# Optimization experiments

Hardware: AMD Instinct MI355X
Metric: run time of the kernel (lower is better)

The kernel has to match this reference:

```python
import jax, jax.numpy as jnp
import numpy as np

B, S, D_IN, D_OUT, H = 4, 2048, 768, 768, 12
DH = D_OUT // H


def setup_inputs() -> dict:
    key = jax.random.key(0)
    ks = jax.random.split(key, 6)
    x = jax.random.normal(ks[0], (B, S, D_IN), dtype=jnp.float32)
    # causal mask: True above the diagonal means "masked out" (filled with -inf)
    mask = jnp.triu(jnp.ones((S, S), dtype=bool), k=1)
    sc = 1.0 / np.sqrt(D_IN)
    Wq = jax.random.normal(ks[1], (D_IN, D_OUT), dtype=jnp.float32) * sc
    Wk = jax.random.normal(ks[2], (D_IN, D_OUT), dtype=jnp.float32) * sc
    Wv = jax.random.normal(ks[3], (D_IN, D_OUT), dtype=jnp.float32) * sc
    Wo = jax.random.normal(ks[4], (D_OUT, D_OUT), dtype=jnp.float32) * (1.0 / np.sqrt(D_OUT))
    bo = jnp.zeros((D_OUT,), dtype=jnp.float32)
    return {"input_tensor": x, "mask": mask, "Wq": Wq, "Wk": Wk, "Wv": Wv, "Wo": Wo, "bo": bo}


def reference(input_tensor, mask, Wq, Wk, Wv, Wo, bo):
    b, n, _ = input_tensor.shape
    # projections -> [b, h, n, dh]
    q = (input_tensor @ Wq).reshape(b, n, H, DH).transpose(0, 2, 1, 3)
    k = (input_tensor @ Wk).reshape(b, n, H, DH).transpose(0, 2, 1, 3)
    v = (input_tensor @ Wv).reshape(b, n, H, DH).transpose(0, 2, 1, 3)
    # scores [b, h, n, n]
    scores = jnp.einsum('bhqd,bhkd->bhqk', q, k)
    scores = jnp.where(mask[:n, :n], -jnp.inf, scores)
    attn = jax.nn.softmax(scores / np.sqrt(DH), axis=-1)
    ctx = jnp.einsum('bhqk,bhkd->bhqd', attn, v)
    ctx = ctx.transpose(0, 2, 1, 3).reshape(b, n, D_OUT)
    return ctx @ Wo + bo
```

## Files before the change

kernel.cpp:

```cpp
#include <hip/hip_runtime.h>
#include <hip/hip_bf16.h>
#include <math.h>

typedef __attribute__((ext_vector_type(4))) float f32x4;
typedef __attribute__((ext_vector_type(8))) short s16x8;
typedef __attribute__((ext_vector_type(8))) unsigned short u16x8;

#define B_ 4
#define S_ 2048
#define DIN 768
#define DOUT 768
#define H_ 12
#define DH_ 64
#define M_ (B_*S_)

__device__ __forceinline__ unsigned short f2bf(float f) {
  union { float f; unsigned u; } v; v.f = f;
  unsigned r = v.u + 0x7fffu + ((v.u >> 16) & 1u);
  return (unsigned short)(r >> 16);
}


__global__ __launch_bounds__(256) void prep(
    const float* __restrict__ X, unsigned short* __restrict__ Xb,
    const float* __restrict__ W0, const float* __restrict__ W1,
    const float* __restrict__ W2, const float* __restrict__ W3,
    unsigned short* __restrict__ Wt)
{
  __shared__ float t[32][33];
  const int bid = blockIdx.x;
  if (bid < 3072) {
    size_t i = ((size_t)bid * 256 + threadIdx.x) * 8;
    float4 a = *(const float4*)&X[i];
    float4 b = *(const float4*)&X[i + 4];
    u16x8 v;
    v[0] = f2bf(a.x); v[1] = f2bf(a.y); v[2] = f2bf(a.z); v[3] = f2bf(a.w);
    v[4] = f2bf(b.x); v[5] = f2bf(b.y); v[6] = f2bf(b.z); v[7] = f2bf(b.w);
    *(u16x8*)&Xb[i] = v;
  } else {
    const int t4 = bid - 3072;
    const int z = t4 / 576, rem = t4 - z * 576;
    const int ky = rem / 24, nx = rem - ky * 24;
    const float* W = z == 0 ? W0 : z == 1 ? W1 : z == 2 ? W2 : W3;
    unsigned short* Out = Wt + (size_t)z * DOUT * DIN;
    const int n0 = nx * 32, k0 = ky * 32;
    const int tx = threadIdx.x & 31, ty = threadIdx.x >> 5;
#pragma unroll
    for (int i = 0; i < 32; i += 8)
      t[ty + i][tx] = W[(size_t)(k0 + ty + i) * DOUT + n0 + tx];
    __syncthreads();
#pragma unroll
    for (int i = 0; i < 32; i += 8)
      Out[(size_t)(n0 + ty + i) * DIN + k0 + tx] = f2bf(t[tx][ty + i]);
  }
}


#define BKC 64
#define TILE_E (128 * BKC)

__device__ __forceinline__ void stage_tile(
    const unsigned short* __restrict__ g, int row0, int k0,
    unsigned short* lds, int tid)
{
#pragma unroll
  for (int it = 0; it < 4; ++it) {
    int s = it * 256 + tid;
    int row = s >> 3, sc = s & 7;
    int gc = sc ^ (row & 7);
    const unsigned short* gsrc = g + (size_t)(row0 + row) * 768 + k0 + gc * 8;
    unsigned short* dst = lds + (size_t)(it * 256 + (tid & ~63)) * 8;
    __builtin_amdgcn_global_load_lds(
        (const __attribute__((address_space(1))) void*)gsrc,
        (__attribute__((address_space(3))) void*)dst, 16, 0, 0);
  }
}

__device__ __forceinline__ void gemm_core(
    const unsigned short* __restrict__ A, const unsigned short* __restrict__ Bt,
    int m0, int n0, unsigned short* As, unsigned short* Bs,
    f32x4 acc[4][4], int tid)
{
  const int lane = tid & 63;
  const int col_l = lane & 15, quad = lane >> 4;
  const int w = tid >> 6;
  const int wm = (w & 1) * 64, wn = (w >> 1) * 64;

  stage_tile(A, m0, 0, As, tid);
  stage_tile(Bt, n0, 0, Bs, tid);

#pragma unroll 2
  for (int k0 = 0; k0 < 768; k0 += BKC) {
    const int cur = (k0 >> 6) & 1;
    const unsigned short* Asb = As + cur * TILE_E;
    const unsigned short* Bsb = Bs + cur * TILE_E;
    if (k0 + BKC < 768) {
      stage_tile(A, m0, k0 + BKC, As + (cur ^ 1) * TILE_E, tid);
      stage_tile(Bt, n0, k0 + BKC, Bs + (cur ^ 1) * TILE_E, tid);
      asm volatile("s_waitcnt vmcnt(8)" ::: "memory");
    } else {
      asm volatile("s_waitcnt vmcnt(0)" ::: "memory");
    }
    __builtin_amdgcn_s_barrier();

#pragma unroll
    for (int kk = 0; kk < 2; ++kk) {
      s16x8 af[4], bf[4];
#pragma unroll
      for (int t = 0; t < 4; ++t) {
        int ar = wm + t * 16 + col_l;
        af[t] = *(const s16x8*)&Asb[ar * BKC + (((kk << 2) + quad) ^ (ar & 7)) * 8];
        int br = wn + t * 16 + col_l;
        bf[t] = *(const s16x8*)&Bsb[br * BKC + (((kk << 2) + quad) ^ (br & 7)) * 8];
      }
#pragma unroll
      for (int mt = 0; mt < 4; ++mt)
#pragma unroll
        for (int nt = 0; nt < 4; ++nt)
          acc[mt][nt] = __builtin_amdgcn_mfma_f32_16x16x32_bf16(
              af[mt], bf[nt], acc[mt][nt], 0, 0, 0);
    }

    __builtin_amdgcn_s_barrier();
  }
}

__global__ __launch_bounds__(256) void proj_mfma(
    const unsigned short* __restrict__ Xb, const unsigned short* __restrict__ Wt,
    unsigned short* __restrict__ Qo, unsigned short* __restrict__ Ko,
    unsigned short* __restrict__ Vo)
{
  __shared__ unsigned short As[2 * TILE_E];
  __shared__ unsigned short Bs[2 * TILE_E];
  const int tid = threadIdx.x;

  const int orig = (blockIdx.z * 64 + blockIdx.y) * 6 + blockIdx.x;
  const int id = (orig & 7) * 144 + (orig >> 3);
  const int z = id / 384;
  const int r = id - z * 384;
  const int my = r / 6, nx = r - my * 6;
  const int m0 = my * 128, n0 = nx * 128;

  const unsigned short* Bw = Wt + (size_t)z * DOUT * DIN;
  unsigned short* Out = z == 0 ? Qo : z == 1 ? Ko : Vo;
  const float scale = z == 0 ? 0.125f : 1.0f;

  f32x4 acc[4][4] = {};
  gemm_core(Xb, Bw, m0, n0, As, Bs, acc, tid);

  const int lane = tid & 63, w = tid >> 6;
  const int col_l = lane & 15, quad = lane >> 4;
  const int wm = (w & 1) * 64, wn = (w >> 1) * 64;
  if (z == 2) {
    const int mblk = m0 + wm;
    const int b = mblk >> 11, sblk = mblk & (S_ - 1);
#pragma unroll
    for (int mt = 0; mt < 4; ++mt) {
      const int slot = (mt >> 1) * 32 + quad * 8 + (mt & 1) * 4;
#pragma unroll
      for (int nt = 0; nt < 4; ++nt) {
        int n = n0 + wn + nt * 16 + col_l;
        int h = n >> 6, d = n & 63;
        ushort4 v;
        v.x = f2bf(acc[mt][nt][0]); v.y = f2bf(acc[mt][nt][1]);
        v.z = f2bf(acc[mt][nt][2]); v.w = f2bf(acc[mt][nt][3]);
        *(ushort4*)&Out[((size_t)(b * H_ + h) * DH_ + d) * S_ + sblk + slot] = v;
      }
    }
  } else {
#pragma unroll
    for (int mt = 0; mt < 4; ++mt)
#pragma unroll
      for (int nt = 0; nt < 4; ++nt) {
        int n = n0 + wn + nt * 16 + col_l;
        int h = n >> 6, d = n & 63;
#pragma unroll
        for (int r2 = 0; r2 < 4; ++r2) {
          int m = m0 + wm + mt * 16 + quad * 4 + r2;
          int b = m >> 11, s = m & (S_ - 1);
          Out[((size_t)(b * H_ + h) * S_ + s) * DH_ + d] = f2bf(acc[mt][nt][r2] * scale);
        }
      }
  }
}

__global__ __launch_bounds__(256) void out_mfma(
    const unsigned short* __restrict__ Cb, const unsigned short* __restrict__ Wt,
    const float* __restrict__ bo, float* __restrict__ Out)
{
  __shared__ unsigned short As[2 * TILE_E];
  __shared__ unsigned short Bs[2 * TILE_E];
  const int tid = threadIdx.x;

  const int orig = blockIdx.y * 6 + blockIdx.x;
  const int id = (orig & 7) * 48 + (orig >> 3);
  const int my = id / 6, nx = id - my * 6;
  const int m0 = my * 128, n0 = nx * 128;

  f32x4 acc[4][4] = {};
  gemm_core(Cb, Wt, m0, n0, As, Bs, acc, tid);

  const int lane = tid & 63, w = tid >> 6;
  const int col_l = lane & 15, quad = lane >> 4;
  const int wm = (w & 1) * 64, wn = (w >> 1) * 64;
#pragma unroll
  for (int mt = 0; mt < 4; ++mt)
#pragma unroll
    for (int nt = 0; nt < 4; ++nt) {
      int n = n0 + wn + nt * 16 + col_l;
      float bias = bo[n];
#pragma unroll
      for (int r = 0; r < 4; ++r) {
        int m = m0 + wm + mt * 16 + quad * 4 + r;
        Out[(size_t)m * DOUT + n] = acc[mt][nt][r] + bias;
      }
    }
}


#define KSTR 72

union PK { uint2 u2[2]; s16x8 v; };

#define MFMA_BF16 __builtin_amdgcn_mfma_f32_16x16x32_bf16

__device__ __forceinline__ void exppack(const f32x4 sc[4], PK& p0, PK& p1) {
#pragma unroll
  for (int nc = 0; nc < 4; ++nc) {
    float e0 = __expf(sc[nc][0] - 12.0f);
    float e1 = __expf(sc[nc][1] - 12.0f);
    float e2 = __expf(sc[nc][2] - 12.0f);
    float e3 = __expf(sc[nc][3] - 12.0f);
    union { __hip_bfloat162 v; unsigned u; } lo, hi;
    lo.v = __float22bfloat162_rn(make_float2(e0, e1));
    hi.v = __float22bfloat162_rn(make_float2(e2, e3));
    uint2 pw; pw.x = lo.u; pw.y = hi.u;
    if (nc < 2) p0.u2[nc] = pw; else p1.u2[nc - 2] = pw;
  }
}

__global__ __launch_bounds__(256, 3) void attn_mfma(
    const unsigned short* __restrict__ Q, const unsigned short* __restrict__ K,
    const unsigned short* __restrict__ Vt, unsigned short* __restrict__ CTX)
{
  __shared__ unsigned short Ks[2][64 * KSTR];
  __shared__ unsigned short Vs[2][64 * KSTR];

  const int tid = threadIdx.x;
  const int lane = tid & 63;
  const int w = tid >> 6;
  const int col_l = lane & 15;
  const int quad = lane >> 4;

  const int orig = (blockIdx.z * 12 + blockIdx.y) * 16 + blockIdx.x;
  const int id = (orig & 7) * 96 + (orig >> 3);
  const int p = id & 15;
  const int bh = id >> 4;
  const int h = bh % 12, b = bh / 12;

  const int q0A = p << 6, q0B = (31 - p) << 6;
  const int ntiles = 32 - p;
  const size_t bhs = (size_t)(b * H_ + h);
  const unsigned short* Qg = Q + bhs * S_ * DH_;
  const unsigned short* Kg = K + bhs * S_ * DH_;
  const unsigned short* Vg = Vt + bhs * DH_ * S_;

  const int qwA = q0A + (w << 4), qwB = q0B + (w << 4);
  s16x8 aqA0 = *(const s16x8*)&Qg[(size_t)(qwA + col_l) * DH_ + quad * 8];
  s16x8 aqA1 = *(const s16x8*)&Qg[(size_t)(qwA + col_l) * DH_ + 32 + quad * 8];
  s16x8 aqB0 = *(const s16x8*)&Qg[(size_t)(qwB + col_l) * DH_ + quad * 8];
  s16x8 aqB1 = *(const s16x8*)&Qg[(size_t)(qwB + col_l) * DH_ + 32 + quad * 8];

  const int krow = lane;
  const int vrow = tid >> 3;
  const int vslot = tid & 7;

  s16x8 kp0 = *(const s16x8*)&Kg[(size_t)krow * DH_ + w * 8];
  s16x8 kp1 = *(const s16x8*)&Kg[(size_t)krow * DH_ + (w + 4) * 8];
  s16x8 vp0 = *(const s16x8*)&Vg[(size_t)vrow * S_ + vslot * 8];
  s16x8 vp1 = *(const s16x8*)&Vg[(size_t)(vrow + 32) * S_ + vslot * 8];

  f32x4 oA[4] = {}, oB[4] = {}, lA = {}, lB = {};
  s16x8 bones;
#pragma unroll
  for (int i = 0; i < 8; ++i) bones[i] = (short)0x3F80;

  const int qrel = (w << 4) + col_l;

  for (int t = 0; t < ntiles; ++t) {
    unsigned short* KsB = &Ks[t & 1][0];
    unsigned short* VsB = &Vs[t & 1][0];
    *(s16x8*)&KsB[krow * KSTR + w * 8] = kp0;
    *(s16x8*)&KsB[krow * KSTR + (w + 4) * 8] = kp1;
    *(s16x8*)&VsB[vrow * KSTR + vslot * 8] = vp0;
    *(s16x8*)&VsB[(vrow + 32) * KSTR + vslot * 8] = vp1;
    __syncthreads();
    {
      const int jn = (t + 1 < ntiles ? t + 1 : t) << 6;
      kp0 = *(const s16x8*)&Kg[(size_t)(jn + krow) * DH_ + w * 8];
      kp1 = *(const s16x8*)&Kg[(size_t)(jn + krow) * DH_ + (w + 4) * 8];
      vp0 = *(const s16x8*)&Vg[(size_t)vrow * S_ + jn + vslot * 8];
      vp1 = *(const s16x8*)&Vg[(size_t)(vrow + 32) * S_ + jn + vslot * 8];
    }
    const bool doA = (t <= p);

    f32x4 scA[4], scB[4];
#pragma unroll
    for (int nc = 0; nc < 4; ++nc) {
      s16x8 k0 = *(const s16x8*)&KsB[(nc * 16 + col_l) * KSTR + quad * 8];
      s16x8 k1 = *(const s16x8*)&KsB[(nc * 16 + col_l) * KSTR + 32 + quad * 8];
      f32x4 a = {};
      a = MFMA_BF16(k0, aqB0, a, 0, 0, 0);
      a = MFMA_BF16(k1, aqB1, a, 0, 0, 0);
      scB[nc] = a;
      if (doA) {
        f32x4 c = {};
        c = MFMA_BF16(k0, aqA0, c, 0, 0, 0);
        c = MFMA_BF16(k1, aqA1, c, 0, 0, 0);
        scA[nc] = c;
      }
    }
    if (t == p) {
#pragma unroll
      for (int nc = 0; nc < 4; ++nc)
#pragma unroll
        for (int r = 0; r < 4; ++r)
          if (nc * 16 + quad * 4 + r > qrel) scA[nc][r] = -INFINITY;
    }
    if (t == ntiles - 1) {
#pragma unroll
      for (int nc = 0; nc < 4; ++nc)
#pragma unroll
        for (int r = 0; r < 4; ++r)
          if (nc * 16 + quad * 4 + r > qrel) scB[nc][r] = -INFINITY;
    }

    PK pA0, pA1, pB0, pB1;
    if (doA) exppack(scA, pA0, pA1);
    exppack(scB, pB0, pB1);

#pragma unroll
    for (int dc = 0; dc < 4; ++dc) {
      s16x8 b0 = *(const s16x8*)&VsB[(dc * 16 + col_l) * KSTR + quad * 8];
      s16x8 b1 = *(const s16x8*)&VsB[(dc * 16 + col_l) * KSTR + 32 + quad * 8];
      oB[dc] = MFMA_BF16(pB0.v, b0, oB[dc], 0, 0, 0);
      oB[dc] = MFMA_BF16(pB1.v, b1, oB[dc], 0, 0, 0);
      if (doA) {
        oA[dc] = MFMA_BF16(pA0.v, b0, oA[dc], 0, 0, 0);
        oA[dc] = MFMA_BF16(pA1.v, b1, oA[dc], 0, 0, 0);
      }
    }
    lB = MFMA_BF16(pB0.v, bones, lB, 0, 0, 0);
    lB = MFMA_BF16(pB1.v, bones, lB, 0, 0, 0);
    if (doA) {
      lA = MFMA_BF16(pA0.v, bones, lA, 0, 0, 0);
      lA = MFMA_BF16(pA1.v, bones, lA, 0, 0, 0);
    }
  }

  float liA[4], liB[4];
#pragma unroll
  for (int r = 0; r < 4; ++r) {
    liA[r] = 1.0f / lA[r];
    liB[r] = 1.0f / lB[r];
  }
#pragma unroll
  for (int dc = 0; dc < 4; ++dc)
#pragma unroll
    for (int r = 0; r < 4; ++r) {
      CTX[((size_t)(b * S_ + qwA + quad * 4 + r)) * DOUT + h * DH_ + dc * 16 + col_l]
          = f2bf(oA[dc][r] * liA[r]);
      CTX[((size_t)(b * S_ + qwB + quad * 4 + r)) * DOUT + h * DH_ + dc * 16 + col_l]
          = f2bf(oB[dc][r] * liB[r]);
    }
}


extern "C" void kernel_launch(void* const* d_in, const int* in_sizes, int n_in,
                              void* d_out, int out_size, void* d_ws, size_t ws_size,
                              hipStream_t stream) {
  const float* X  = (const float*)d_in[0];
  const float* Wq = (const float*)d_in[2];
  const float* Wk = (const float*)d_in[3];
  const float* Wv = (const float*)d_in[4];
  const float* Wo = (const float*)d_in[5];
  const float* bo = (const float*)d_in[6];
  float* out = (float*)d_out;

  unsigned short* Xb = (unsigned short*)d_ws;
  unsigned short* Wt = Xb + (size_t)M_ * DIN;
  unsigned short* Qb = Wt + (size_t)4 * DOUT * DIN;
  unsigned short* Kb = Qb + (size_t)M_ * DOUT;
  unsigned short* Vb = Kb + (size_t)M_ * DOUT;
  unsigned short* Cb = Vb + (size_t)M_ * DOUT;

  prep<<<dim3(3072 + 2304), 256, 0, stream>>>(X, Xb, Wq, Wk, Wv, Wo, Wt);
  proj_mfma<<<dim3(DOUT / 128, M_ / 128, 3), 256, 0, stream>>>(Xb, Wt, Qb, Kb, Vb);
  attn_mfma<<<dim3(16, H_, B_), 256, 0, stream>>>(Qb, Kb, Vb, Cb);
  out_mfma<<<dim3(DOUT / 128, M_ / 128), 256, 0, stream>>>(
      Cb, Wt + (size_t)3 * DOUT * DIN, bo, out);
}
```

Before: 197.9 us.

## Load K directly to registers, stage V via async global-to-LDS with swizzle

The attention kernel stops staging K in LDS. Each wave now loads its K fragments straight from global memory into registers. V is staged with direct global_load_lds into an unpadded, XOR-swizzled LDS buffer and prefetched one tile ahead, using explicit vmcnt waits and raw barriers. Q is prescaled by log2(e) so the softmax can use the native exp2, and s_setprio is raised around the MFMA sections. This cuts LDS traffic and register staging, but every wave re-reads K from global or L2, and correctness now depends on hand-written waitcnt counts.

```diff
diff --git a/kernel.cpp b/kernel.cpp
--- a/kernel.cpp
+++ b/kernel.cpp
@@ -19,6 +19,12 @@
   unsigned r = v.u + 0x7fffu + ((v.u >> 16) & 1u);
   return (unsigned short)(r >> 16);
 }
+
+#if __has_builtin(__builtin_amdgcn_exp2f)
+#define EXP2(x) __builtin_amdgcn_exp2f(x)
+#else
+#define EXP2(x) exp2f(x)
+#endif
 
 
 __global__ __launch_bounds__(256) void prep(
@@ -143,7 +149,7 @@
 
   const unsigned short* Bw = Wt + (size_t)z * DOUT * DIN;
   unsigned short* Out = z == 0 ? Qo : z == 1 ? Ko : Vo;
-  const float scale = z == 0 ? 0.125f : 1.0f;
+  const float scale = z == 0 ? 0.125f * 1.44269504f : 1.0f;
 
   f32x4 acc[4][4] = {};
   gemm_core(Xb, Bw, m0, n0, As, Bs, acc, tid);
@@ -218,8 +224,6 @@
 }
 
 
-#define KSTR 72
-
 union PK { uint2 u2[2]; s16x8 v; };
 
 #define MFMA_BF16 __builtin_amdgcn_mfma_f32_16x16x32_bf16
@@ -227,10 +231,10 @@
 __device__ __forceinline__ void exppack(const f32x4 sc[4], PK& p0, PK& p1) {
 #pragma unroll
   for (int nc = 0; nc < 4; ++nc) {
-    float e0 = __expf(sc[nc][0] - 12.0f);
-    float e1 = __expf(sc[nc][1] - 12.0f);
-    float e2 = __expf(sc[nc][2] - 12.0f);
-    float e3 = __expf(sc[nc][3] - 12.0f);
+    float e0 = EXP2(sc[nc][0] - 17.3123405f);
+    float e1 = EXP2(sc[nc][1] - 17.3123405f);
+    float e2 = EXP2(sc[nc][2] - 17.3123405f);
+    float e3 = EXP2(sc[nc][3] - 17.3123405f);
     union { __hip_bfloat162 v; unsigned u; } lo, hi;
     lo.v = __float22bfloat162_rn(make_float2(e0, e1));
     hi.v = __float22bfloat162_rn(make_float2(e2, e3));
@@ -239,12 +243,27 @@
   }
 }
 
+__device__ __forceinline__ void stage_v(
+    const unsigned short* __restrict__ g, int jn,
+    unsigned short* lds, int tid)
+{
+#pragma unroll
+  for (int it = 0; it < 2; ++it) {
+    int s = it * 256 + tid;
+    int row = s >> 3, c = s & 7;
+    const unsigned short* gsrc = g + (size_t)row * S_ + jn + ((c ^ (row & 7)) * 8);
+    unsigned short* dst = lds + (size_t)(it * 256 + (tid & ~63)) * 8;
+    __builtin_amdgcn_global_load_lds(
+        (const __attribute__((address_space(1))) void*)gsrc,
+        (__attribute__((address_space(3))) void*)dst, 16, 0, 0);
+  }
+}
+
 __global__ __launch_bounds__(256, 3) void attn_mfma(
     const unsigned short* __restrict__ Q, const unsigned short* __restrict__ K,
     const unsigned short* __restrict__ Vt, unsigned short* __restrict__ CTX)
 {
-  __shared__ unsigned short Ks[2][64 * KSTR];
-  __shared__ unsigned short Vs[2][64 * KSTR];
+  __shared__ unsigned short Vs[2][64 * 64];
 
   const int tid = threadIdx.x;
   const int lane = tid & 63;
@@ -271,14 +290,7 @@
   s16x8 aqB0 = *(const s16x8*)&Qg[(size_t)(qwB + col_l) * DH_ + quad * 8];
   s16x8 aqB1 = *(const s16x8*)&Qg[(size_t)(qwB + col_l) * DH_ + 32 + quad * 8];
 
-  const int krow = lane;
-  const int vrow = tid >> 3;
-  const int vslot = tid & 7;
-
-  s16x8 kp0 = *(const s16x8*)&Kg[(size_t)krow * DH_ + w * 8];
-  s16x8 kp1 = *(const s16x8*)&Kg[(size_t)krow * DH_ + (w + 4) * 8];
-  s16x8 vp0 = *(const s16x8*)&Vg[(size_t)vrow * S_ + vslot * 8];
-  s16x8 vp1 = *(const s16x8*)&Vg[(size_t)(vrow + 32) * S_ + vslot * 8];
+  stage_v(Vg, 0, &Vs[0][0], tid);
 
   f32x4 oA[4] = {}, oB[4] = {}, lA = {}, lB = {};
   s16x8 bones;
@@ -286,40 +298,39 @@
   for (int i = 0; i < 8; ++i) bones[i] = (short)0x3F80;
 
   const int qrel = (w << 4) + col_l;
+  const int r7 = col_l & 7;
 
   for (int t = 0; t < ntiles; ++t) {
-    unsigned short* KsB = &Ks[t & 1][0];
-    unsigned short* VsB = &Vs[t & 1][0];
-    *(s16x8*)&KsB[krow * KSTR + w * 8] = kp0;
-    *(s16x8*)&KsB[krow * KSTR + (w + 4) * 8] = kp1;
-    *(s16x8*)&VsB[vrow * KSTR + vslot * 8] = vp0;
-    *(s16x8*)&VsB[(vrow + 32) * KSTR + vslot * 8] = vp1;
-    __syncthreads();
-    {
-      const int jn = (t + 1 < ntiles ? t + 1 : t) << 6;
-      kp0 = *(const s16x8*)&Kg[(size_t)(jn + krow) * DH_ + w * 8];
-      kp1 = *(const s16x8*)&Kg[(size_t)(jn + krow) * DH_ + (w + 4) * 8];
-      vp0 = *(const s16x8*)&Vg[(size_t)vrow * S_ + jn + vslot * 8];
-      vp1 = *(const s16x8*)&Vg[(size_t)(vrow + 32) * S_ + jn + vslot * 8];
-    }
+    __builtin_amdgcn_s_barrier();
+
+    const int j = t << 6;
+    s16x8 k0f[4], k1f[4];
+#pragma unroll
+    for (int nc = 0; nc < 4; ++nc) {
+      const unsigned short* kr = &Kg[(size_t)(j + nc * 16 + col_l) * DH_ + quad * 8];
+      k0f[nc] = *(const s16x8*)kr;
+      k1f[nc] = *(const s16x8*)(kr + 32);
+    }
+    if (t + 1 < ntiles) stage_v(Vg, (t + 1) << 6, &Vs[(t + 1) & 1][0], tid);
+
     const bool doA = (t <= p);
 
     f32x4 scA[4], scB[4];
+    __builtin_amdgcn_s_setprio(1);
 #pragma unroll
     for (int nc = 0; nc < 4; ++nc) {
-      s16x8 k0 = *(const s16x8*)&KsB[(nc * 16 + col_l) * KSTR + quad * 8];
-      s16x8 k1 = *(const s16x8*)&KsB[(nc * 16 + col_l) * KSTR + 32 + quad * 8];
       f32x4 a = {};
-      a = MFMA_BF16(k0, aqB0, a, 0, 0, 0);
-      a = MFMA_BF16(k1, aqB1, a, 0, 0, 0);
+      a = MFMA_BF16(k0f[nc], aqB0, a, 0, 0, 0);
+      a = MFMA_BF16(k1f[nc], aqB1, a, 0, 0, 0);
       scB[nc] = a;
       if (doA) {
         f32x4 c = {};
-        c = MFMA_BF16(k0, aqA0, c, 0, 0, 0);
-        c = MFMA_BF16(k1, aqA1, c, 0, 0, 0);
+        c = MFMA_BF16(k0f[nc], aqA0, c, 0, 0, 0);
+        c = MFMA_BF16(k1f[nc], aqA1, c, 0, 0, 0);
         scA[nc] = c;
       }
     }
+    __builtin_amdgcn_s_setprio(0);
     if (t == p) {
 #pragma unroll
       for (int nc = 0; nc < 4; ++nc)
@@ -339,10 +350,19 @@
     if (doA) exppack(scA, pA0, pA1);
     exppack(scB, pB0, pB1);
 
+    __builtin_amdgcn_sched_barrier(0);
+    if (t + 1 < ntiles) asm volatile("s_waitcnt vmcnt(2)" ::: "memory");
+    else                asm volatile("s_waitcnt vmcnt(0)" ::: "memory");
+    __builtin_amdgcn_s_barrier();
+    __builtin_amdgcn_sched_barrier(0);
+
+    const unsigned short* VsB = &Vs[t & 1][0];
+    __builtin_amdgcn_s_setprio(1);
 #pragma unroll
     for (int dc = 0; dc < 4; ++dc) {
-      s16x8 b0 = *(const s16x8*)&VsB[(dc * 16 + col_l) * KSTR + quad * 8];
-      s16x8 b1 = *(const s16x8*)&VsB[(dc * 16 + col_l) * KSTR + 32 + quad * 8];
+      const int row = dc * 16 + col_l;
+      s16x8 b0 = *(const s16x8*)&VsB[row * 64 + ((quad ^ r7) * 8)];
+      s16x8 b1 = *(const s16x8*)&VsB[row * 64 + (((quad + 4) ^ r7) * 8)];
       oB[dc] = MFMA_BF16(pB0.v, b0, oB[dc], 0, 0, 0);
       oB[dc] = MFMA_BF16(pB1.v, b1, oB[dc], 0, 0, 0);
       if (doA) {
@@ -356,6 +376,7 @@
       lA = MFMA_BF16(pA0.v, bones, lA, 0, 0, 0);
       lA = MFMA_BF16(pA1.v, bones, lA, 0, 0, 0);
     }
+    __builtin_amdgcn_s_setprio(0);
   }
 
   float liA[4], liB[4];
```

New measurement: 249.3 us. +26.0%, slower.
